# Performance work log

Hardware: AMD Instinct MI355X
Metric: run time of the kernel (lower is better)

## Reference

```python
import jax, jax.numpy as jnp
import numpy as np

S = 30.0   # scale
M = 0.3    # additive angular margin (arcface)
EPS = 1e-07


def setup_inputs() -> dict:
    key = jax.random.key(0)
    k1, k2, k3 = jax.random.split(key, 3)
    N, D, C = 8192, 256, 10000
    x = jax.random.normal(k1, (N, D), dtype=jnp.float32)
    W = jax.random.normal(k2, (C, D), dtype=jnp.float32) * 0.05  # linear weight [C, D]
    target = jax.random.randint(k3, (N,), 0, C)
    return {"x": x, "W": W, "target": target}


def reference(x, W, target):
    # L2-normalize inputs along features. NOTE: the torch code's loop that
    # 'normalizes' weight_fc params is a no-op (rebinds a local), so W is
    # intentionally NOT normalized here, matching the original math.
    xn = x / jnp.linalg.norm(x, axis=1, keepdims=True)
    logits = xn @ W.T                                   # [N, C]
    n = logits.shape[0]
    tgt = logits[jnp.arange(n), target]                 # [N] target-class cosine-like score
    # arcface margin: s * cos(acos(clamp(t)) + m)
    numerator = S * jnp.cos(jnp.arccos(jnp.clip(tgt, -1.0 + EPS, 1.0 - EPS)) + M)
    # exclude-target sum: sum_j exp(s*logits) minus the target column (no [N,C-1] concat)
    exp_s = jnp.exp(S * logits)                         # [N, C]
    sum_excl = jnp.sum(exp_s, axis=1) - jnp.exp(S * tgt)
    denominator = jnp.exp(numerator) + sum_excl
    L = numerator - jnp.log(denominator)
    return -jnp.mean(L)
```

## Files before the change

### kernel.cpp

```cpp
#include <hip/hip_runtime.h>
#include <hip/hip_bf16.h>
#include <stdint.h>

#define S_SCALE 30.0f
#define A_QSCALE 2.70505320166681f
#define N_ROWS 8192
#define D_DIM 256
#define C_CLS 10000
#define NCB 8

typedef __attribute__((ext_vector_type(4))) float f32x4;

static __device__ __forceinline__ void gl16(const void* g, void* l) {
  __builtin_amdgcn_global_load_lds(
      (const __attribute__((address_space(1))) void*)g,
      (__attribute__((address_space(3))) void*)l, 16, 0, 0);
}

static __device__ __forceinline__ long u2l(uint2 v) {
  union { uint2 u; long l; } x; x.u = v; return x.l;
}

static __device__ __forceinline__ float row_sum16(float v) {
  union { float f; int i; } u, w;
  u.f = v;
  w.i = __builtin_amdgcn_update_dpp(0, u.i, 0xB1, 0xF, 0xF, true);  u.f += w.f;
  w.i = __builtin_amdgcn_update_dpp(0, u.i, 0x4E, 0xF, 0xF, true);  u.f += w.f;
  w.i = __builtin_amdgcn_update_dpp(0, u.i, 0x141, 0xF, 0xF, true); u.f += w.f;
  w.i = __builtin_amdgcn_update_dpp(0, u.i, 0x140, 0xF, 0xF, true); u.f += w.f;
  return u.f;
}

__global__ __launch_bounds__(256) void k_prep(const float* __restrict__ x,
                                              const float* __restrict__ W,
                                              const int* __restrict__ target,
                                              unsigned char* __restrict__ xnb8,
                                              unsigned char* __restrict__ WbF8,
                                              float* __restrict__ tgt) {
  if (blockIdx.x < 1280) {
    int gidx = blockIdx.x * 256 + threadIdx.x;
    int lane = gidx & 63;
    int kc = (gidx >> 6) & 7;
    int c16 = gidx >> 9;
    int col = c16 * 16 + (lane & 15);
    int k0 = kc * 32 + (lane >> 4) * 8;
    int r0 = 0, r1 = 0;
    if (col < C_CLS) {
      const float4 a = *(const float4*)(W + (size_t)col * D_DIM + k0);
      const float4 b = *(const float4*)(W + (size_t)col * D_DIM + k0 + 4);
      r0 = __builtin_amdgcn_cvt_pk_fp8_f32(a.x * 16.f, a.y * 16.f, 0, false);
      r0 = __builtin_amdgcn_cvt_pk_fp8_f32(a.z * 16.f, a.w * 16.f, r0, true);
      r1 = __builtin_amdgcn_cvt_pk_fp8_f32(b.x * 16.f, b.y * 16.f, 0, false);
      r1 = __builtin_amdgcn_cvt_pk_fp8_f32(b.z * 16.f, b.w * 16.f, r1, true);
    }
    *(int2*)(WbF8 + (size_t)gidx * 8) = (int2){r0, r1};
  } else {
    int row = (blockIdx.x - 1280) * 4 + (threadIdx.x >> 6);
    int l = threadIdx.x & 63;
    const float4 v = *(const float4*)(x + (size_t)row * D_DIM + l * 4);
    float ss = v.x * v.x + v.y * v.y + v.z * v.z + v.w * v.w;
#pragma unroll
    for (int m = 1; m < 64; m <<= 1) ss += __shfl_xor(ss, m, 64);
    float rn = 1.0f / sqrtf(ss);
    float s8 = rn * A_QSCALE;
    int r0 = __builtin_amdgcn_cvt_pk_fp8_f32(v.x * s8, v.y * s8, 0, false);
    r0 = __builtin_amdgcn_cvt_pk_fp8_f32(v.z * s8, v.w * s8, r0, true);
    int panel = row >> 7, r16 = (row >> 4) & 7, lr = row & 15;
    size_t dst = (size_t)panel * 32768 + (size_t)(r16 * 8 + (l >> 3)) * 512 +
                 (size_t)(((l >> 1) & 3) * 16 + lr) * 8 + (l & 1) * 4;
    *(int*)(xnb8 + dst) = r0;
    int tc = target[row];
    const float4 b = *(const float4*)(W + (size_t)tc * D_DIM + l * 4);
    float s = v.x * b.x + v.y * b.y + v.z * b.z + v.w * b.w;
#pragma unroll
    for (int m = 1; m < 64; m <<= 1) s += __shfl_xor(s, m, 64);
    if (l == 0) tgt[row] = s * rn;
  }
}

__global__ __launch_bounds__(512, 4) void k_gemm(const unsigned char* __restrict__ xnb8,
                                                 const unsigned char* __restrict__ WbF8,
                                                 float* __restrict__ partials) {
  __shared__ __align__(16) char lds[34816];
  const int b = blockIdx.x;
  const int cg = b & 7;
  const int br = b >> 3;
  const int bc0 = cg * 5;
  const int t = threadIdx.x;
  const int w = t >> 6, l = t & 63;
  const int wr = w >> 2, wc = w & 3;
  const int lr = l & 15, lk = l >> 4;
  float* rsumAll = (float*)(lds + 32768);

  if (t < 512) rsumAll[t] = 0.f;

  {
    const char* Ag = (const char*)xnb8 + (size_t)br * 32768;
#pragma unroll
    for (int i = 0; i < 4; ++i)
      gl16(Ag + i * 8192 + w * 1024 + l * 16, lds + i * 8192 + w * 1024);
    asm volatile("s_waitcnt vmcnt(0)" ::: "memory");
    __builtin_amdgcn_sched_barrier(0);
    __builtin_amdgcn_s_barrier();
  }

  f32x4 acc[4][4];
  const f32x4 z4 = (f32x4){0.f, 0.f, 0.f, 0.f};

  const char* AwL = lds + (size_t)(wr * 4 * 8) * 512 + (size_t)l * 8;
  const unsigned char* Bw = WbF8 + (size_t)(bc0 * 16 + wc * 4) * 4096 + (size_t)l * 8;
  float* rw = rsumAll + w * 64;

  uint2 b0[4], b1[4];
#pragma unroll
  for (int fn = 0; fn < 4; ++fn) b0[fn] = *(const uint2*)(Bw + fn * 4096);

  for (int tt = 0; tt < 5; ++tt) {
    auto step = [&](int kc, bool first, uint2(&cur)[4], uint2(&nxt)[4]) {
      if (kc < 7) {
#pragma unroll
        for (int fn = 0; fn < 4; ++fn)
          nxt[fn] = *(const uint2*)(Bw + fn * 4096 + (kc + 1) * 512);
      } else if (tt < 4) {
#pragma unroll
        for (int fn = 0; fn < 4; ++fn)
          nxt[fn] = *(const uint2*)(Bw + 65536 + fn * 4096);
      }
      __builtin_amdgcn_s_setprio(1);
#pragma unroll
      for (int fm = 0; fm < 4; ++fm) {
        long a = u2l(*(const uint2*)(AwL + (fm * 8 + kc) * 512));
#pragma unroll
        for (int fn = 0; fn < 4; ++fn)
          acc[fm][fn] = __builtin_amdgcn_mfma_f32_16x16x32_fp8_fp8(
              a, u2l(cur[fn]), first ? z4 : acc[fm][fn], 0, 0, 0);
      }
      __builtin_amdgcn_s_setprio(0);
    };
    step(0, true, b0, b1);  step(1, false, b1, b0);
    step(2, false, b0, b1); step(3, false, b1, b0);
    step(4, false, b0, b1); step(5, false, b1, b0);
    step(6, false, b0, b1); step(7, false, b1, b0);

#pragma unroll
    for (int m = 0; m < 4; ++m) {
      float rs0 = 0.f, rs1 = 0.f, rs2 = 0.f, rs3 = 0.f;
#pragma unroll
      for (int n = 0; n < 4; ++n) {
        rs0 += __builtin_amdgcn_exp2f(acc[m][n][0]);
        rs1 += __builtin_amdgcn_exp2f(acc[m][n][1]);
        rs2 += __builtin_amdgcn_exp2f(acc[m][n][2]);
        rs3 += __builtin_amdgcn_exp2f(acc[m][n][3]);
      }
      rs0 = row_sum16(rs0); rs1 = row_sum16(rs1);
      rs2 = row_sum16(rs2); rs3 = row_sum16(rs3);
      if (lr == 0) {
        int row = m * 16 + lk * 4;
        rw[row + 0] += rs0; rw[row + 1] += rs1;
        rw[row + 2] += rs2; rw[row + 3] += rs3;
      }
    }
    Bw += 65536;
  }

  __syncthreads();
  if (t < 128) {
    int wr2 = t >> 6, r = t & 63;
    float sv = rsumAll[(wr2 * 4 + 0) * 64 + r] + rsumAll[(wr2 * 4 + 1) * 64 + r] +
               rsumAll[(wr2 * 4 + 2) * 64 + r] + rsumAll[(wr2 * 4 + 3) * 64 + r];
    partials[(size_t)cg * N_ROWS + (size_t)br * 128 + t] = sv;
  }
}

__global__ __launch_bounds__(256) void k_loss1(const float* __restrict__ partials,
                                               const float* __restrict__ tgt,
                                               float* __restrict__ bsum) {
  __shared__ float wsum[4];
  int i = blockIdx.x * 256 + threadIdx.x;
  const float* p = partials + i;
  float s = -240.0f;
#pragma unroll
  for (int j = 0; j < NCB; ++j) s += p[(size_t)j * N_ROWS];
  float tl = tgt[i];
  float tcv = fminf(fmaxf(tl, -1.0f + 1e-7f), 1.0f - 1e-7f);
  const float cm = 0.95533648912560601964f;
  const float sm = 0.29552020666133957510f;
  float num = S_SCALE * (tcv * cm - sqrtf(fmaxf(1.0f - tcv * tcv, 0.f)) * sm);
  float sum_excl = s - __expf(S_SCALE * tl);
  float denom = __expf(num) + sum_excl;
  float L = num - __logf(denom);
#pragma unroll
  for (int m = 1; m < 64; m <<= 1) L += __shfl_xor(L, m, 64);
  int l = threadIdx.x & 63, w = threadIdx.x >> 6;
  if (l == 0) wsum[w] = L;
  __syncthreads();
  if (threadIdx.x == 0) bsum[blockIdx.x] = wsum[0] + wsum[1] + wsum[2] + wsum[3];
}

__global__ void k_loss2(const float* __restrict__ bsum, float* __restrict__ out) {
  float s = 0.f;
  for (int i = 0; i < 32; ++i) s += bsum[i];
  out[0] = -s / (float)N_ROWS;
}

extern "C" void kernel_launch(void* const* d_in, const int* in_sizes, int n_in,
                              void* d_out, int out_size, void* d_ws, size_t ws_size,
                              hipStream_t stream) {
  const float* x = (const float*)d_in[0];
  const float* W = (const float*)d_in[1];
  const int* target = (const int*)d_in[2];
  float* out = (float*)d_out;
  char* ws = (char*)d_ws;

  unsigned char* xnb8 = (unsigned char*)(ws);
  unsigned char* WbF8 = (unsigned char*)(ws + 2097152);
  float* tgt = (float*)(ws + 4718592);
  float* partials = (float*)(ws + 4751360);
  float* bsum = (float*)(ws + 5013504);

  k_prep<<<3328, 256, 0, stream>>>(x, W, target, xnb8, WbF8, tgt);
  k_gemm<<<512, 512, 0, stream>>>(xnb8, WbF8, partials);
  k_loss1<<<32, 256, 0, stream>>>(partials, tgt, bsum);
  k_loss2<<<1, 1, 0, stream>>>(bsum, out);
}
```

Before: 48.65 us.

## Switch GEMM from fp8 MFMA to int8 16x16x64 MFMA with new layouts

Quantizes normalized x and W to symmetric int8 with fixed scales instead of fp8, and re-lays out both operands so each lane holds 16 contiguous bytes per 64-wide K chunk. The GEMM uses the i32 16x16x64 int8 MFMA, halving the instruction count per K step, and the epilogue converts the int accumulators to float with a combined scale before exp2. The register double-buffered B prefetch is dropped in favor of loading B right before each K window, which may expose global load latency. Fixed quantization scales also risk clipping and loss of precision compared with fp8.

```diff
diff --git a/kernel.cpp b/kernel.cpp
--- a/kernel.cpp
+++ b/kernel.cpp
@@ -3,13 +3,15 @@
 #include <stdint.h>
 
 #define S_SCALE 30.0f
-#define A_QSCALE 2.70505320166681f
+#define XSC 360.0f
+#define WSC 400.0f
+#define SC_EPI 3.00561467e-4f
 #define N_ROWS 8192
 #define D_DIM 256
 #define C_CLS 10000
 #define NCB 8
 
-typedef __attribute__((ext_vector_type(4))) float f32x4;
+typedef __attribute__((ext_vector_type(4))) int i32x4;
 
 static __device__ __forceinline__ void gl16(const void* g, void* l) {
   __builtin_amdgcn_global_load_lds(
@@ -17,8 +19,12 @@
       (__attribute__((address_space(3))) void*)l, 16, 0, 0);
 }
 
-static __device__ __forceinline__ long u2l(uint2 v) {
-  union { uint2 u; long l; } x; x.u = v; return x.l;
+static __device__ __forceinline__ int q4(float a, float b, float c, float d) {
+  int qa = (int)rintf(fminf(fmaxf(a, -127.f), 127.f));
+  int qb = (int)rintf(fminf(fmaxf(b, -127.f), 127.f));
+  int qc = (int)rintf(fminf(fmaxf(c, -127.f), 127.f));
+  int qd = (int)rintf(fminf(fmaxf(d, -127.f), 127.f));
+  return (qa & 255) | ((qb & 255) << 8) | ((qc & 255) << 16) | ((qd & 255) << 24);
 }
 
 static __device__ __forceinline__ float row_sum16(float v) {
@@ -39,21 +45,22 @@
                                               float* __restrict__ tgt) {
   if (blockIdx.x < 1280) {
     int gidx = blockIdx.x * 256 + threadIdx.x;
-    int lane = gidx & 63;
-    int kc = (gidx >> 6) & 7;
+    int sub = gidx & 1;
+    int lane = (gidx >> 1) & 63;
+    int kchunk = (gidx >> 7) & 3;
     int c16 = gidx >> 9;
     int col = c16 * 16 + (lane & 15);
-    int k0 = kc * 32 + (lane >> 4) * 8;
+    int k0 = kchunk * 64 + (lane >> 4) * 16 + sub * 8;
     int r0 = 0, r1 = 0;
     if (col < C_CLS) {
       const float4 a = *(const float4*)(W + (size_t)col * D_DIM + k0);
       const float4 b = *(const float4*)(W + (size_t)col * D_DIM + k0 + 4);
-      r0 = __builtin_amdgcn_cvt_pk_fp8_f32(a.x * 16.f, a.y * 16.f, 0, false);
-      r0 = __builtin_amdgcn_cvt_pk_fp8_f32(a.z * 16.f, a.w * 16.f, r0, true);
-      r1 = __builtin_amdgcn_cvt_pk_fp8_f32(b.x * 16.f, b.y * 16.f, 0, false);
-      r1 = __builtin_amdgcn_cvt_pk_fp8_f32(b.z * 16.f, b.w * 16.f, r1, true);
+      r0 = q4(a.x * WSC, a.y * WSC, a.z * WSC, a.w * WSC);
+      r1 = q4(b.x * WSC, b.y * WSC, b.z * WSC, b.w * WSC);
     }
-    *(int2*)(WbF8 + (size_t)gidx * 8) = (int2){r0, r1};
+    size_t dst = (size_t)c16 * 4096 + (size_t)kchunk * 1024 +
+                 (size_t)lane * 16 + (size_t)sub * 8;
+    *(int2*)(WbF8 + dst) = (int2){r0, r1};
   } else {
     int row = (blockIdx.x - 1280) * 4 + (threadIdx.x >> 6);
     int l = threadIdx.x & 63;
@@ -62,12 +69,14 @@
 #pragma unroll
     for (int m = 1; m < 64; m <<= 1) ss += __shfl_xor(ss, m, 64);
     float rn = 1.0f / sqrtf(ss);
-    float s8 = rn * A_QSCALE;
-    int r0 = __builtin_amdgcn_cvt_pk_fp8_f32(v.x * s8, v.y * s8, 0, false);
-    r0 = __builtin_amdgcn_cvt_pk_fp8_f32(v.z * s8, v.w * s8, r0, true);
+    float s8 = rn * XSC;
+    int r0 = q4(v.x * s8, v.y * s8, v.z * s8, v.w * s8);
     int panel = row >> 7, r16 = (row >> 4) & 7, lr = row & 15;
-    size_t dst = (size_t)panel * 32768 + (size_t)(r16 * 8 + (l >> 3)) * 512 +
-                 (size_t)(((l >> 1) & 3) * 16 + lr) * 8 + (l & 1) * 4;
+    int kchunk = l >> 4;
+    int lk = (l >> 2) & 3;
+    int byte = (l & 3) * 4;
+    size_t dst = (size_t)panel * 32768 + (size_t)(r16 * 4 + kchunk) * 1024 +
+                 (size_t)(lk * 16 + lr) * 16 + byte;
     *(int*)(xnb8 + dst) = r0;
     int tc = target[row];
     const float4 b = *(const float4*)(W + (size_t)tc * D_DIM + l * 4);
@@ -104,53 +113,43 @@
     __builtin_amdgcn_s_barrier();
   }
 
-  f32x4 acc[4][4];
-  const f32x4 z4 = (f32x4){0.f, 0.f, 0.f, 0.f};
-
-  const char* AwL = lds + (size_t)(wr * 4 * 8) * 512 + (size_t)l * 8;
-  const unsigned char* Bw = WbF8 + (size_t)(bc0 * 16 + wc * 4) * 4096 + (size_t)l * 8;
+  i32x4 acc[4][4];
+  const i32x4 zi = (i32x4){0, 0, 0, 0};
+
+  const char* AwL = lds + (size_t)wr * 16384 + (size_t)l * 16;
+  const unsigned char* Bw = WbF8 + (size_t)(bc0 * 16 + wc * 4) * 4096 + (size_t)l * 16;
   float* rw = rsumAll + w * 64;
 
-  uint2 b0[4], b1[4];
-#pragma unroll
-  for (int fn = 0; fn < 4; ++fn) b0[fn] = *(const uint2*)(Bw + fn * 4096);
-
   for (int tt = 0; tt < 5; ++tt) {
-    auto step = [&](int kc, bool first, uint2(&cur)[4], uint2(&nxt)[4]) {
-      if (kc < 7) {
+    const unsigned char* Bt = Bw + (size_t)tt * 65536;
+
+    auto windw = [&](int kc, bool first) {
+      i32x4 bf[4];
+#pragma unroll
+      for (int fn = 0; fn < 4; ++fn)
+        bf[fn] = *(const i32x4*)(Bt + fn * 4096 + kc * 1024);
+      __builtin_amdgcn_s_setprio(1);
+#pragma unroll
+      for (int fm = 0; fm < 4; ++fm) {
+        i32x4 a = *(const i32x4*)(AwL + (fm * 4 + kc) * 1024);
 #pragma unroll
         for (int fn = 0; fn < 4; ++fn)
-          nxt[fn] = *(const uint2*)(Bw + fn * 4096 + (kc + 1) * 512);
-      } else if (tt < 4) {
-#pragma unroll
-        for (int fn = 0; fn < 4; ++fn)
-          nxt[fn] = *(const uint2*)(Bw + 65536 + fn * 4096);
-      }
-      __builtin_amdgcn_s_setprio(1);
-#pragma unroll
-      for (int fm = 0; fm < 4; ++fm) {
-        long a = u2l(*(const uint2*)(AwL + (fm * 8 + kc) * 512));
-#pragma unroll
-        for (int fn = 0; fn < 4; ++fn)
-          acc[fm][fn] = __builtin_amdgcn_mfma_f32_16x16x32_fp8_fp8(
-              a, u2l(cur[fn]), first ? z4 : acc[fm][fn], 0, 0, 0);
+          acc[fm][fn] = __builtin_amdgcn_mfma_i32_16x16x64_i8(
+              a, bf[fn], first ? zi : acc[fm][fn], 0, 0, 0);
       }
       __builtin_amdgcn_s_setprio(0);
     };
-    step(0, true, b0, b1);  step(1, false, b1, b0);
-    step(2, false, b0, b1); step(3, false, b1, b0);
-    step(4, false, b0, b1); step(5, false, b1, b0);
-    step(6, false, b0, b1); step(7, false, b1, b0);
+    windw(0, true); windw(1, false); windw(2, false); windw(3, false);
 
 #pragma unroll
     for (int m = 0; m < 4; ++m) {
       float rs0 = 0.f, rs1 = 0.f, rs2 = 0.f, rs3 = 0.f;
 #pragma unroll
       for (int n = 0; n < 4; ++n) {
-        rs0 += __builtin_amdgcn_exp2f(acc[m][n][0]);
-        rs1 += __builtin_amdgcn_exp2f(acc[m][n][1]);
-        rs2 += __builtin_amdgcn_exp2f(acc[m][n][2]);
-        rs3 += __builtin_amdgcn_exp2f(acc[m][n][3]);
+        rs0 += __builtin_amdgcn_exp2f((float)acc[m][n][0] * SC_EPI);
+        rs1 += __builtin_amdgcn_exp2f((float)acc[m][n][1] * SC_EPI);
+        rs2 += __builtin_amdgcn_exp2f((float)acc[m][n][2] * SC_EPI);
+        rs3 += __builtin_amdgcn_exp2f((float)acc[m][n][3] * SC_EPI);
       }
       rs0 = row_sum16(rs0); rs1 = row_sum16(rs1);
       rs2 = row_sum16(rs2); rs3 = row_sum16(rs3);
@@ -160,7 +159,6 @@
         rw[row + 2] += rs2; rw[row + 3] += rs3;
       }
     }
-    Bw += 65536;
   }
 
   __syncthreads();
```

After: 44.10 us, median of 2. -9.3%, faster.
